# Performance work log

Measured on AMD Instinct MI355X. Metric: run time of the kernel, lower is better.

## Reference

```python
import jax, jax.numpy as jnp
import numpy as np

NUM_FEATURES = 512
NUM_HEADS = 8
DIM_PER_HEAD = NUM_FEATURES // NUM_HEADS


def setup_inputs() -> dict:
    key = jax.random.key(0)
    ks = jax.random.split(key, 9)
    B, C, H, W = 8, NUM_FEATURES, 32, 32
    # xavier_uniform bound for 1x1 conv: sqrt(6/(fan_in+fan_out)) = sqrt(6/(2C))
    bound = float(np.sqrt(6.0 / (2.0 * C)))
    # conv bias default init: U(-1/sqrt(fan_in), 1/sqrt(fan_in))
    bbound = float(1.0 / np.sqrt(C))
    return {
        "query": jax.random.normal(ks[0], (B, C, H, W), jnp.float32),
        "key": jax.random.normal(ks[1], (B, C, H, W), jnp.float32),
        "value": jax.random.normal(ks[2], (B, C, H, W), jnp.float32),
        "wq": jax.random.uniform(ks[3], (C, C), jnp.float32, -bound, bound),
        "bq": jax.random.uniform(ks[4], (C,), jnp.float32, -bbound, bbound),
        "wk": jax.random.uniform(ks[5], (C, C), jnp.float32, -bound, bound),
        "bk": jax.random.uniform(ks[6], (C,), jnp.float32, -bbound, bbound),
        "wv": jax.random.uniform(ks[7], (C, C), jnp.float32, -bound, bound),
        "bv": jax.random.uniform(ks[8], (C,), jnp.float32, -bbound, bbound),
    }


def _proj(x, w, b):
    # 1x1 conv == per-pixel linear over channels. x: [B,C,H,W], w: [Cout,Cin]
    return jnp.einsum('oi,bihw->bohw', w, x) + b[None, :, None, None]


def _split_heads(x, nh, d):
    B, C, H, W = x.shape
    # view (B, nh, d, H*W) then permute -> (B, nh, S, d)
    return x.reshape(B, nh, d, H * W).transpose(0, 1, 3, 2)


def reference(query, key, value, wq, bq, wk, bk, wv, bv):
    B, C, H, W = query.shape
    nh, d = NUM_HEADS, DIM_PER_HEAD
    q = _split_heads(_proj(query, wq, bq), nh, d)   # [B,nh,S,d]
    k = _split_heads(_proj(key, wk, bk), nh, d)
    v = _split_heads(_proj(value, wv, bv), nh, d)
    scores = jnp.einsum('bhsd,bhtd->bhst', q, k) / jnp.sqrt(jnp.float32(d))
    attn = jax.nn.softmax(scores, axis=-1)          # [B,nh,S,S]
    out = jnp.einsum('bhst,bhtd->bhsd', attn, v)    # [B,nh,S,d]
    # combine_heads (faithful to torch): permute to (B,S,nh,d), flat reshape
    out = out.transpose(0, 2, 1, 3)                 # [B,S,nh,d]
    return out.reshape(B, C, H, W)
```

## Files before the change

### kernel.cpp

```cpp
#include <hip/hip_runtime.h>
#include <hip/hip_bf16.h>
#include <stdint.h>


typedef __attribute__((ext_vector_type(4))) float f32x4;
typedef __attribute__((ext_vector_type(8))) short short8;

#define GLB_AS(p) ((const __attribute__((address_space(1))) void*)(p))
#define LDS_AS(p) ((__attribute__((address_space(3))) void*)(p))

__device__ __forceinline__ unsigned short f2b(float f) {
  unsigned int x = __builtin_bit_cast(unsigned int, f);
  x = (x + 0x7FFFu + ((x >> 16) & 1u)) >> 16;
  return (unsigned short)x;
}

__device__ __forceinline__ unsigned short f2b_fast(float f) {
  unsigned int x = __builtin_bit_cast(unsigned int, f);
  return (unsigned short)((x + 0x8000u) >> 16);
}

__device__ __forceinline__ float exp2_hw(float x) {
  float r;
  asm("v_exp_f32 %0, %1" : "=v"(r) : "v"(x));
  return r;
}

__device__ __forceinline__ f32x4 mfma16(short8 a, short8 b, f32x4 c) {
  return __builtin_amdgcn_mfma_f32_16x16x32_bf16(a, b, c, 0, 0, 0);
}

__global__ __launch_bounds__(256) void transpose_cast3(const float* __restrict__ Xq,
                                                       const float* __restrict__ Xk,
                                                       const float* __restrict__ Xv,
                                                       unsigned short* __restrict__ Xt) {
  __shared__ float t[64][65];
  const int which = blockIdx.z >> 3, bb = blockIdx.z & 7;
  const float* X = (which == 0) ? Xq : ((which == 1) ? Xk : Xv);
  const int s0 = blockIdx.x * 64, c0 = blockIdx.y * 64;
  const float* Xb = X + (long)bb * 512 * 1024;
  const int tid = threadIdx.x;
  const int col4 = (tid & 15) * 4;
  const int r0 = tid >> 4;
#pragma unroll
  for (int it = 0; it < 4; ++it) {
    int r = r0 + it * 16;
    const float4 v = *(const float4*)&Xb[(long)(c0 + r) * 1024 + s0 + col4];
    t[r][col4 + 0] = v.x; t[r][col4 + 1] = v.y; t[r][col4 + 2] = v.z; t[r][col4 + 3] = v.w;
  }
  __syncthreads();
  const int s = tid >> 2;
  const int cp = (tid & 3) * 16;
  unsigned int u[8];
#pragma unroll
  for (int i = 0; i < 8; ++i) {
    unsigned int lo = f2b(t[cp + 2 * i][s]);
    unsigned int hi = f2b(t[cp + 2 * i + 1][s]);
    u[i] = lo | (hi << 16);
  }
  unsigned short* dst = Xt + (long)which * 8 * 1024 * 512 +
                        ((long)bb * 1024 + s0 + s) * 512 + c0 + cp;
  ((uint4*)dst)[0] = make_uint4(u[0], u[1], u[2], u[3]);
  ((uint4*)dst)[1] = make_uint4(u[4], u[5], u[6], u[7]);
}

__global__ __launch_bounds__(256) void cast_w3(const float* __restrict__ wq,
                                               const float* __restrict__ wk,
                                               const float* __restrict__ wv,
                                               unsigned short* __restrict__ O) {
  const int y = blockIdx.y;
  const float* W = (y == 0) ? wq : ((y == 1) ? wk : wv);
  int i = blockIdx.x * 256 + threadIdx.x;
  float4 v = ((const float4*)W)[i];
  uint2 u;
  u.x = (unsigned)f2b(v.x) | ((unsigned)f2b(v.y) << 16);
  u.y = (unsigned)f2b(v.z) | ((unsigned)f2b(v.w) << 16);
  ((uint2*)(O + (long)y * 262144))[i] = u;
}

__global__ __launch_bounds__(256, 2) void gemm_proj(
    const unsigned short* __restrict__ XT, const unsigned short* __restrict__ W3,
    unsigned short* __restrict__ QKV, const float* __restrict__ bq,
    const float* __restrict__ bk, const float* __restrict__ bv) {
  __shared__ __align__(16) unsigned short lA[128 * 64];
  __shared__ __align__(16) unsigned short lB[128 * 64];
  const long SC = 1024L * 512;
  const int bid = blockIdx.x;
  const int kind = bid >> 8;
  const int rr = bid & 255;
  const int batch = rr >> 5, tile = rr & 31;
  const unsigned short *Ab, *Bb;
  unsigned short* Cb;
  const float* bias;
  int m0, n0, N, biasN;
  float scale = 1.0f;
  if (kind < 2) {
    m0 = (tile >> 2) * 128; n0 = (tile & 3) * 128; N = 512; biasN = 1;
    Ab = XT + ((long)kind * 8 + batch) * SC;
    Bb = W3 + (long)kind * 262144;
    Cb = QKV + ((long)kind * 8 + batch) * SC;
    bias = kind ? bk : bq;
    if (kind == 0) scale = 0.18033688011112042f;
  } else {
    m0 = (tile >> 3) * 128; n0 = (tile & 7) * 128; N = 1024; biasN = 0;
    Ab = W3 + 2 * 262144;
    Bb = XT + (16L + batch) * SC;
    Cb = QKV + (16L + batch) * SC;
    bias = bv;
  }
  const int tid = threadIdx.x, lane = tid & 63, wid = tid >> 6;
  const int wr = wid >> 1, wc = wid & 1;
  const int lm = lane & 15, lg = lane >> 4;
  f32x4 acc[4][4] = {};
  for (int k0 = 0; k0 < 512; k0 += 64) {
#pragma unroll
    for (int ch = wid; ch < 16; ch += 4) {
      int e = ch * 512 + lane * 8;
      int r = e >> 6, cc = e & 63;
      __builtin_amdgcn_global_load_lds(GLB_AS(Ab + (long)(m0 + r) * 512 + k0 + cc),
                                       LDS_AS(lA + ch * 512), 16, 0, 0);
      __builtin_amdgcn_global_load_lds(GLB_AS(Bb + (long)(n0 + r) * 512 + k0 + cc),
                                       LDS_AS(lB + ch * 512), 16, 0, 0);
    }
    __syncthreads();
#pragma unroll
    for (int kk = 0; kk < 2; ++kk) {
      short8 af[4], bf[4];
#pragma unroll
      for (int i = 0; i < 4; ++i)
        af[i] = *(const short8*)&lA[(wr * 64 + i * 16 + lm) * 64 + kk * 32 + 8 * lg];
#pragma unroll
      for (int j = 0; j < 4; ++j)
        bf[j] = *(const short8*)&lB[(wc * 64 + j * 16 + lm) * 64 + kk * 32 + 8 * lg];
#pragma unroll
      for (int i = 0; i < 4; ++i)
#pragma unroll
        for (int j = 0; j < 4; ++j)
          acc[i][j] = mfma16(af[i], bf[j], acc[i][j]);
    }
    __syncthreads();
  }
#pragma unroll
  for (int i = 0; i < 4; ++i)
#pragma unroll
    for (int j = 0; j < 4; ++j)
#pragma unroll
      for (int r = 0; r < 4; ++r) {
        int m = m0 + wr * 64 + i * 16 + lg * 4 + r;
        int n = n0 + wc * 64 + j * 16 + lm;
        float bvv = biasN ? bias[n] : bias[m];
        Cb[(long)m * N + n] = f2b((acc[i][j][r] + bvv) * scale);
      }
}

__global__ __launch_bounds__(256, 2) void attn(
    const unsigned short* __restrict__ Qt, const unsigned short* __restrict__ Kt,
    const unsigned short* __restrict__ V, float* __restrict__ Out) {
  __shared__ __align__(16) unsigned short lK[2][64 * 64];
  __shared__ __align__(16) unsigned short lV[2][64 * 64];
  __shared__ __align__(16) unsigned short Pl[4][32][72];
  const int flat = blockIdx.x;
  const int xcd = flat & 7, j = flat >> 3;
  const int pair = xcd * 8 + (j >> 3);
  const int st = j & 7;
  const int b = pair >> 3, h = pair & 7;
  const int tid = threadIdx.x, lane = tid & 63, w = tid >> 6;
  const int lm = lane & 15, lg = lane >> 4;
  const int s0 = st * 128 + w * 32;
  const unsigned short* Qb = Qt + ((long)b * 1024 + s0) * 512 + h * 64;
  const unsigned short* Kb = Kt + (long)b * 1024 * 512 + h * 64;
  const unsigned short* Vb = V + ((long)b * 512 + h * 64) * 1024;

  const int srow = (w << 1) * 8 + (lane >> 3);
  const int scol = ((lane & 7) ^ (lane >> 3)) * 8;
  auto stage = [&](int buf, int t0) {
#pragma unroll
    for (int jj = 0; jj < 2; ++jj) {
      int ch = (w << 1) + jj;
      int row = srow + jj * 8;
      __builtin_amdgcn_global_load_lds(GLB_AS(Kb + (long)(t0 + row) * 512 + scol),
                                       LDS_AS(&lK[buf][ch * 512]), 16, 0, 0);
      __builtin_amdgcn_global_load_lds(GLB_AS(Vb + (long)row * 1024 + t0 + scol),
                                       LDS_AS(&lV[buf][ch * 512]), 16, 0, 0);
    }
  };

  short8 qf[2][2];
#pragma unroll
  for (int si = 0; si < 2; ++si)
#pragma unroll
    for (int kk = 0; kk < 2; ++kk)
      qf[si][kk] = *(const short8*)&Qb[(si * 16 + lm) * 512 + kk * 32 + 8 * lg];

  f32x4 o[2][4] = {};
  float lsum[2][4] = {};

  stage(0, 0);
  __syncthreads();

#pragma unroll 1
  for (int t = 0; t < 16; ++t) {
    const int cur = t & 1;
    if (t < 15) stage(cur ^ 1, (t + 1) * 64);
    f32x4 s[2][4] = {};
    __builtin_amdgcn_s_setprio(1);
#pragma unroll
    for (int tj = 0; tj < 4; ++tj) {
      short8 kf0 = *(const short8*)&lK[cur][(tj * 16 + lm) * 64 + 8 * (lg ^ (lm & 7))];
      short8 kf1 = *(const short8*)&lK[cur][(tj * 16 + lm) * 64 + 8 * ((lg + 4) ^ (lm & 7))];
#pragma unroll
      for (int si = 0; si < 2; ++si) {
        s[si][tj] = mfma16(qf[si][0], kf0, s[si][tj]);
        s[si][tj] = mfma16(qf[si][1], kf1, s[si][tj]);
      }
    }
    __builtin_amdgcn_s_setprio(0);
#pragma unroll
    for (int si = 0; si < 2; ++si)
#pragma unroll
      for (int tj = 0; tj < 4; ++tj)
#pragma unroll
        for (int r = 0; r < 4; ++r) {
          float p = exp2_hw(s[si][tj][r]);
          s[si][tj][r] = p;
          lsum[si][r] += p;
        }
#pragma unroll
    for (int si = 0; si < 2; ++si)
#pragma unroll
      for (int tj = 0; tj < 4; ++tj)
#pragma unroll
        for (int r = 0; r < 4; ++r)
          Pl[w][si * 16 + lg * 4 + r][tj * 16 + lm] = f2b_fast(s[si][tj][r]);
    __builtin_amdgcn_s_setprio(1);
#pragma unroll
    for (int tk = 0; tk < 2; ++tk) {
      short8 pa0 = *(const short8*)&Pl[w][lm][tk * 32 + 8 * lg];
      short8 pa1 = *(const short8*)&Pl[w][16 + lm][tk * 32 + 8 * lg];
#pragma unroll
      for (int dj = 0; dj < 4; ++dj) {
        short8 vf = *(const short8*)&lV[cur][(dj * 16 + lm) * 64 + 8 * ((tk * 4 + lg) ^ (lm & 7))];
        o[0][dj] = mfma16(pa0, vf, o[0][dj]);
        o[1][dj] = mfma16(pa1, vf, o[1][dj]);
      }
    }
    __builtin_amdgcn_s_setprio(0);
    __syncthreads();
  }

  float inv[2][4];
#pragma unroll
  for (int si = 0; si < 2; ++si)
#pragma unroll
    for (int r = 0; r < 4; ++r) {
      float rs = lsum[si][r];
      rs += __shfl_xor(rs, 1);
      rs += __shfl_xor(rs, 2);
      rs += __shfl_xor(rs, 4);
      rs += __shfl_xor(rs, 8);
      inv[si][r] = 1.0f / rs;
    }
#pragma unroll
  for (int si = 0; si < 2; ++si)
#pragma unroll
    for (int dj = 0; dj < 4; ++dj)
#pragma unroll
      for (int r = 0; r < 4; ++r) {
        int srow2 = s0 + si * 16 + lg * 4 + r;
        Out[((long)b * 1024 + srow2) * 512 + h * 64 + dj * 16 + lm] = o[si][dj][r] * inv[si][r];
      }
}

extern "C" void kernel_launch(void* const* d_in, const int* in_sizes, int n_in,
                              void* d_out, int out_size, void* d_ws, size_t ws_size,
                              hipStream_t stream) {
  const float* query = (const float*)d_in[0];
  const float* key   = (const float*)d_in[1];
  const float* value = (const float*)d_in[2];
  const float* wq = (const float*)d_in[3];
  const float* bq = (const float*)d_in[4];
  const float* wk = (const float*)d_in[5];
  const float* bk = (const float*)d_in[6];
  const float* wv = (const float*)d_in[7];
  const float* bv = (const float*)d_in[8];

  unsigned short* ws = (unsigned short*)d_ws;
  const long SC = 1024L * 512;
  unsigned short* XT  = ws;
  unsigned short* W3  = XT + 24 * SC;
  unsigned short* QKV = W3 + 3 * 262144;
  unsigned short* QT  = QKV;
  unsigned short* KTm = QKV + 8 * SC;
  unsigned short* VVm = QKV + 16 * SC;

  transpose_cast3<<<dim3(16, 8, 24), 256, 0, stream>>>(query, key, value, XT);
  cast_w3<<<dim3(256, 3), 256, 0, stream>>>(wq, wk, wv, W3);
  gemm_proj<<<768, 256, 0, stream>>>(XT, W3, QKV, bq, bk, bv);
  attn<<<512, 256, 0, stream>>>(QT, KTm, VVm, (float*)d_out);
}
```

Before: 71.55 us.

## Keep softmax probabilities in registers via transposed QK^T and lane permutes

```diff
diff --git a/kernel.cpp b/kernel.cpp
--- a/kernel.cpp
+++ b/kernel.cpp
@@ -5,6 +5,7 @@
 
 typedef __attribute__((ext_vector_type(4))) float f32x4;
 typedef __attribute__((ext_vector_type(8))) short short8;
+typedef __attribute__((ext_vector_type(4))) unsigned int u32x4;
 
 #define GLB_AS(p) ((const __attribute__((address_space(1))) void*)(p))
 #define LDS_AS(p) ((__attribute__((address_space(3))) void*)(p))
@@ -15,14 +16,15 @@
   return (unsigned short)x;
 }
 
-__device__ __forceinline__ unsigned short f2b_fast(float f) {
-  unsigned int x = __builtin_bit_cast(unsigned int, f);
-  return (unsigned short)((x + 0x8000u) >> 16);
-}
-
 __device__ __forceinline__ float exp2_hw(float x) {
   float r;
   asm("v_exp_f32 %0, %1" : "=v"(r) : "v"(x));
+  return r;
+}
+
+__device__ __forceinline__ unsigned int cvtpk(float lo, float hi) {
+  unsigned int r;
+  asm("v_cvt_pk_bf16_f32 %0, %1, %2" : "=v"(r) : "v"(lo), "v"(hi));
   return r;
 }
 
@@ -158,7 +160,6 @@
     const unsigned short* __restrict__ V, float* __restrict__ Out) {
   __shared__ __align__(16) unsigned short lK[2][64 * 64];
   __shared__ __align__(16) unsigned short lV[2][64 * 64];
-  __shared__ __align__(16) unsigned short Pl[4][32][72];
   const int flat = blockIdx.x;
   const int xcd = flat & 7, j = flat >> 3;
   const int pair = xcd * 8 + (j >> 3);
@@ -193,7 +194,7 @@
       qf[si][kk] = *(const short8*)&Qb[(si * 16 + lm) * 512 + kk * 32 + 8 * lg];
 
   f32x4 o[2][4] = {};
-  float lsum[2][4] = {};
+  float lsum[2] = {};
 
   stage(0, 0);
   __syncthreads();
@@ -210,8 +211,8 @@
       short8 kf1 = *(const short8*)&lK[cur][(tj * 16 + lm) * 64 + 8 * ((lg + 4) ^ (lm & 7))];
 #pragma unroll
       for (int si = 0; si < 2; ++si) {
-        s[si][tj] = mfma16(qf[si][0], kf0, s[si][tj]);
-        s[si][tj] = mfma16(qf[si][1], kf1, s[si][tj]);
+        s[si][tj] = mfma16(kf0, qf[si][0], s[si][tj]);
+        s[si][tj] = mfma16(kf1, qf[si][1], s[si][tj]);
       }
     }
     __builtin_amdgcn_s_setprio(0);
@@ -223,43 +224,53 @@
         for (int r = 0; r < 4; ++r) {
           float p = exp2_hw(s[si][tj][r]);
           s[si][tj][r] = p;
-          lsum[si][r] += p;
+          lsum[si] += p;
         }
 #pragma unroll
-    for (int si = 0; si < 2; ++si)
-#pragma unroll
-      for (int tj = 0; tj < 4; ++tj)
-#pragma unroll
-        for (int r = 0; r < 4; ++r)
-          Pl[w][si * 16 + lg * 4 + r][tj * 16 + lm] = f2b_fast(s[si][tj][r]);
-    __builtin_amdgcn_s_setprio(1);
-#pragma unroll
     for (int tk = 0; tk < 2; ++tk) {
-      short8 pa0 = *(const short8*)&Pl[w][lm][tk * 32 + 8 * lg];
-      short8 pa1 = *(const short8*)&Pl[w][16 + lm][tk * 32 + 8 * lg];
+      short8 pa[2];
+#pragma unroll
+      for (int si = 0; si < 2; ++si) {
+        unsigned int X01 = cvtpk(s[si][2 * tk][0], s[si][2 * tk][1]);
+        unsigned int X23 = cvtpk(s[si][2 * tk][2], s[si][2 * tk][3]);
+        unsigned int Y01 = cvtpk(s[si][2 * tk + 1][0], s[si][2 * tk + 1][1]);
+        unsigned int Y23 = cvtpk(s[si][2 * tk + 1][2], s[si][2 * tk + 1][3]);
+        asm("v_permlane32_swap_b32 %0, %1" : "+v"(X01), "+v"(Y01));
+        asm("v_permlane32_swap_b32 %0, %1" : "+v"(X23), "+v"(Y23));
+        unsigned int Xs01 = (unsigned)__builtin_amdgcn_ds_swizzle((int)X01, 0x401F);
+        unsigned int Xs23 = (unsigned)__builtin_amdgcn_ds_swizzle((int)X23, 0x401F);
+        unsigned int Ys01 = (unsigned)__builtin_amdgcn_ds_swizzle((int)Y01, 0x401F);
+        unsigned int Ys23 = (unsigned)__builtin_amdgcn_ds_swizzle((int)Y23, 0x401F);
+        const bool b0 = (lane >> 4) & 1;
+        u32x4 pw;
+        pw[0] = b0 ? Ys01 : X01;
+        pw[1] = b0 ? Ys23 : X23;
+        pw[2] = b0 ? Y01 : Xs01;
+        pw[3] = b0 ? Y23 : Xs23;
+        pa[si] = __builtin_bit_cast(short8, pw);
+      }
+      __builtin_amdgcn_s_setprio(1);
 #pragma unroll
       for (int dj = 0; dj < 4; ++dj) {
         short8 vf = *(const short8*)&lV[cur][(dj * 16 + lm) * 64 + 8 * ((tk * 4 + lg) ^ (lm & 7))];
-        o[0][dj] = mfma16(pa0, vf, o[0][dj]);
-        o[1][dj] = mfma16(pa1, vf, o[1][dj]);
-      }
-    }
-    __builtin_amdgcn_s_setprio(0);
+        o[0][dj] = mfma16(pa[0], vf, o[0][dj]);
+        o[1][dj] = mfma16(pa[1], vf, o[1][dj]);
+      }
+      __builtin_amdgcn_s_setprio(0);
+    }
     __syncthreads();
   }
 
   float inv[2][4];
 #pragma unroll
-  for (int si = 0; si < 2; ++si)
-#pragma unroll
-    for (int r = 0; r < 4; ++r) {
-      float rs = lsum[si][r];
-      rs += __shfl_xor(rs, 1);
-      rs += __shfl_xor(rs, 2);
-      rs += __shfl_xor(rs, 4);
-      rs += __shfl_xor(rs, 8);
-      inv[si][r] = 1.0f / rs;
-    }
+  for (int si = 0; si < 2; ++si) {
+    float rs = lsum[si];
+    rs += __shfl_xor(rs, 16);
+    rs += __shfl_xor(rs, 32);
+#pragma unroll
+    for (int r = 0; r < 4; ++r)
+      inv[si][r] = 1.0f / __shfl(rs, lg * 4 + r);
+  }
 #pragma unroll
   for (int si = 0; si < 2; ++si)
 #pragma unroll
```

After: 69.40 us. -3.0%, faster.
